# Kernel optimization log

Hardware: AMD Instinct MI355X
Metric: run time of the kernel (lower is better)

## Reference

```python
import jax, jax.numpy as jnp
import numpy as np

N_NODES = 100000
N_EDGES = 3200000
F_IN = 128
HID = 64
N_CLASS = 40


def _glorot(key, shape):
    fan_in, fan_out = shape[1], shape[0]
    s = jnp.sqrt(6.0 / (fan_in + fan_out))
    return jax.random.uniform(key, shape, jnp.float32, -s, s)


def setup_inputs() -> dict:
    key = jax.random.key(0)
    k = jax.random.split(key, 6)
    x = jax.random.normal(k[0], (N_NODES, F_IN), jnp.float32)
    row = jax.random.randint(k[1], (N_EDGES,), 0, N_NODES)
    # guarantee no self loops so add_remaining_self_loops == append all N loops
    off = jax.random.randint(k[2], (N_EDGES,), 1, N_NODES)
    col = (row + off) % N_NODES
    edge_index = jnp.stack([row, col]).astype(jnp.int64)
    y = jax.random.randint(k[3], (N_NODES,), 0, N_CLASS).astype(jnp.int64)
    W1 = _glorot(k[4], (HID, F_IN))
    b1 = jnp.zeros((HID,), jnp.float32)
    W2 = _glorot(k[5], (N_CLASS, HID))
    b2 = jnp.zeros((N_CLASS,), jnp.float32)
    return {"x": x, "edge_index": edge_index, "y": y,
            "W1": W1, "b1": b1, "W2": W2, "b2": b2}


def _gcn_conv(x, edge_index, W, b, num_nodes):
    # append self loops (weight 1.0), per add_remaining_self_loops
    loops = jnp.arange(num_nodes, dtype=edge_index.dtype)
    row = jnp.concatenate([edge_index[0], loops])
    col = jnp.concatenate([edge_index[1], loops])
    w = jnp.ones(row.shape[0], x.dtype)
    # degree-norm: deg over target idx (flow='source_to_target')
    deg = jax.ops.segment_sum(w, col, num_segments=num_nodes)
    dinv = jnp.where(deg > 0, jax.lax.rsqrt(deg), 0.0)
    norm = dinv[row] * w * dinv[col]           # [E+N]
    h = x @ W.T                                # [N, out]
    msg = norm[:, None] * h[row]               # gather + scale
    out = jax.ops.segment_sum(msg, col, num_segments=num_nodes)  # scatter-add
    return out + b


def reference(x, edge_index, y, W1, b1, W2, b2):
    n = x.shape[0]
    h = jax.nn.relu(_gcn_conv(x, edge_index, W1, b1, n))
    # F.dropout treated as identity (eval / deterministic reference)
    x_out = _gcn_conv(h, edge_index, W2, b2, n)
    logp = jax.nn.log_softmax(x_out, axis=1)
    p = jax.nn.softmax(x_out, axis=1)
    pred = jnp.argmax(x_out, axis=1)
    e1 = pred[edge_index[0]]
    e2 = pred[edge_index[1]]
    lab = y[edge_index[0]] == y[edge_index[1]]
    ratio = jnp.mean(((e1 == e2) == lab).astype(jnp.float32))
    return (logp, p, ratio)
```

## Files before the change

kernel.cpp:

```cpp
#include <hip/hip_runtime.h>
#include <hip/hip_fp16.h>

#define N_NODES 100000
#define N_EDGES 3200000
#define F_IN 128
#define HID 64
#define N_CLASS 40
#define ZROW N_NODES

#define NBUCK 196
#define BSHIFT 9
#define NBLK_A 512
#define CHUNK_A ((N_EDGES + NBLK_A - 1) / NBLK_A)

typedef float f32x2 __attribute__((ext_vector_type(2)));

static __device__ __forceinline__ unsigned char enc_fp8(float v) {
    return (unsigned char)(__builtin_amdgcn_cvt_pk_fp8_f32(v, v, 0, false) & 0xff);
}

static __device__ __forceinline__ uint2 gat8(const unsigned char* base, int byteoff, int seg) {
    return *(const uint2*)(base + ((unsigned)byteoff | (unsigned)(seg << 3)));
}

#define CONS(RAW) do { \
    f32x2 f0 = __builtin_amdgcn_cvt_pk_f32_fp8((int)RAW.x, false); \
    f32x2 f1 = __builtin_amdgcn_cvt_pk_f32_fp8((int)RAW.x, true); \
    f32x2 f2 = __builtin_amdgcn_cvt_pk_f32_fp8((int)RAW.y, false); \
    f32x2 f3 = __builtin_amdgcn_cvt_pk_f32_fp8((int)RAW.y, true); \
    a01 += f0; a23 += f1; a45 += f2; a67 += f3; } while (0)

#define SLOTP(s, G, C) { \
    int ib = bb + 6 + s; \
    int srcr = (ib < mydeg) ? C : zb; \
    uint2 ng = gat8(gsrc, srcr, seg); \
    C = sp[min(bb + 12 + s, mlast)]; \
    __builtin_amdgcn_sched_barrier(0); \
    CONS(G); \
    G = ng; }

#define GATHER_PL(TBL) \
    f32x2 a01 = {0.f, 0.f}, a23 = {0.f, 0.f}, a45 = {0.f, 0.f}, a67 = {0.f, 0.f}; \
    { \
        const unsigned char* gsrc = TBL; \
        const int* sp = srow + myoff; \
        const int zb = ZROW << 6; \
        int nbmax = mydeg; \
        nbmax = max(nbmax, __shfl_xor(nbmax, 8)); \
        nbmax = max(nbmax, __shfl_xor(nbmax, 16)); \
        nbmax = max(nbmax, __shfl_xor(nbmax, 32)); \
        if (nbmax > 0) { \
            int mlast = mydeg > 0 ? mydeg - 1 : 0; \
            uint2 g0 = gat8(gsrc, (0 < mydeg) ? sp[0] : zb, seg); \
            uint2 g1 = gat8(gsrc, (1 < mydeg) ? sp[min(1, mlast)] : zb, seg); \
            uint2 g2 = gat8(gsrc, (2 < mydeg) ? sp[min(2, mlast)] : zb, seg); \
            uint2 g3 = gat8(gsrc, (3 < mydeg) ? sp[min(3, mlast)] : zb, seg); \
            uint2 g4 = gat8(gsrc, (4 < mydeg) ? sp[min(4, mlast)] : zb, seg); \
            uint2 g5 = gat8(gsrc, (5 < mydeg) ? sp[min(5, mlast)] : zb, seg); \
            int c0 = sp[min(6, mlast)],  c1 = sp[min(7, mlast)],  c2 = sp[min(8, mlast)]; \
            int c3 = sp[min(9, mlast)], c4 = sp[min(10, mlast)], c5 = sp[min(11, mlast)]; \
            for (int bb = 0; bb < nbmax; bb += 6) { \
                SLOTP(0, g0, c0) SLOTP(1, g1, c1) SLOTP(2, g2, c2) \
                SLOTP(3, g3, c3) SLOTP(4, g4, c4) SLOTP(5, g5, c5) \
            } \
        } \
         \
        uint2 sg = gat8(gsrc, node << 6, seg); \
        CONS(sg); \
    }

__global__ __launch_bounds__(256) void k_A1(const int* __restrict__ col, int* __restrict__ ghistT) {
    __shared__ int hist[256];
    int t = threadIdx.x;
    hist[t] = 0;
    __syncthreads();
    int e0 = blockIdx.x * CHUNK_A;
    int e1 = e0 + CHUNK_A; if (e1 > N_EDGES) e1 = N_EDGES;
    for (int e = e0 + t; e < e1; e += 256) {
        atomicAdd(&hist[col[e] >> BSHIFT], 1);
    }
    __syncthreads();
    ghistT[t * NBLK_A + blockIdx.x] = hist[t];
}

__global__ __launch_bounds__(256) void k_A2a(const int* __restrict__ ghistT, int* __restrict__ goffT,
                                             int* __restrict__ tot) {
    __shared__ int s[256];
    int b = blockIdx.x, t = threadIdx.x;
    int2 v = ((const int2*)(ghistT + b * NBLK_A))[t];
    int pair = v.x + v.y;
    s[t] = pair;
    __syncthreads();
    for (int d = 1; d < 256; d <<= 1) {
        int o = (t >= d) ? s[t - d] : 0;
        __syncthreads();
        s[t] += o;
        __syncthreads();
    }
    int incl = s[t];
    int excl = incl - pair;
    goffT[b * NBLK_A + 2 * t]     = excl;
    goffT[b * NBLK_A + 2 * t + 1] = excl + v.x;
    if (t == 255) tot[b] = incl;
}

__global__ __launch_bounds__(256) void k_A2b(const int* __restrict__ tot, int* __restrict__ bbase,
                                             int* __restrict__ bend,
                                             unsigned char* __restrict__ h1q,
                                             unsigned char* __restrict__ h2q,
                                             const float* __restrict__ b2, float* __restrict__ pb2) {
    __shared__ int s[256];
    int t = threadIdx.x;
    int v = tot[t];
    s[t] = v;
    __syncthreads();
    for (int d = 1; d < 256; d <<= 1) {
        int o = (t >= d) ? s[t - d] : 0;
        __syncthreads();
        s[t] += o;
        __syncthreads();
    }
    bbase[t] = s[t] - v;
    bend[t] = s[t];
    if (t < 64) h1q[(size_t)ZROW * 64 + t] = 0;
    else if (t < 128) h2q[(size_t)ZROW * 64 + (t - 64)] = 0;
    else if (t < 192) pb2[t - 128] = (t - 128 < N_CLASS) ? b2[t - 128] : 0.f;
}

__global__ __launch_bounds__(256) void k_A3(const int* __restrict__ row, const int* __restrict__ col,
                                            const int* __restrict__ goffT, const int* __restrict__ bbase,
                                            unsigned int* __restrict__ epair) {
    __shared__ int cur[256];
    int t = threadIdx.x;
    cur[t] = goffT[t * NBLK_A + blockIdx.x] + bbase[t];
    __syncthreads();
    int e0 = blockIdx.x * CHUNK_A;
    int e1 = e0 + CHUNK_A; if (e1 > N_EDGES) e1 = N_EDGES;
    for (int e = e0 + t; e < e1; e += 256) {
        int c = col[e];
        int pos = atomicAdd(&cur[c >> BSHIFT], 1);
        epair[pos] = ((unsigned int)(c & 511) << 17) | (unsigned int)row[e];
    }
}

__global__ __launch_bounds__(256) void k_B(const unsigned int* __restrict__ epair,
                                           const int* __restrict__ bbase, const int* __restrict__ bend,
                                           int* __restrict__ off, int* __restrict__ pdeg,
                                           float* __restrict__ dinv, int* __restrict__ srow) {
    __shared__ int h[512];
    __shared__ int psc[256];
    int t = threadIdx.x;
    int b = blockIdx.x;
    int n0 = b << BSHIFT;
    int e0 = bbase[b], e1 = bend[b];
    int pbase = e0 + b * 4096;
    h[t] = 0; h[t + 256] = 0;
    __syncthreads();
    for (int e = e0 + t; e < e1; e += 256) {
        atomicAdd(&h[epair[e] >> 17], 1);
    }
    __syncthreads();
    int a0 = h[2 * t], a1 = h[2 * t + 1];
    int p0 = (a0 + 7) & ~7, p1 = (a1 + 7) & ~7;
    psc[t] = p0 + p1;
    __syncthreads();
    for (int d = 1; d < 256; d <<= 1) {
        int o = (t >= d) ? psc[t - d] : 0;
        __syncthreads();
        psc[t] += o;
        __syncthreads();
    }
    int base0 = pbase + psc[t] - (p0 + p1);
    int base1 = base0 + p0;
    h[2 * t] = base0;
    h[2 * t + 1] = base1;
    int n = n0 + 2 * t;
    const int zb = ZROW << 6;
    if (n < N_NODES) {
        off[n] = base0; pdeg[n] = p0; dinv[n] = rsqrtf((float)a0 + 1.0f);
        for (int p = a0; p < p0; ++p) srow[base0 + p] = zb;
    }
    if (n + 1 < N_NODES) {
        off[n + 1] = base1; pdeg[n + 1] = p1; dinv[n + 1] = rsqrtf((float)a1 + 1.0f);
        for (int p = a1; p < p1; ++p) srow[base1 + p] = zb;
    }
    __syncthreads();
    for (int e = e0 + t; e < e1; e += 256) {
        unsigned int k = epair[e];
        int c = k >> 17;
        int pos = atomicAdd(&h[c], 1);
        srow[pos] = (int)(k & 0x1FFFFu) << 6;
    }
}

__global__ __launch_bounds__(256, 4) void k_gemm1(const float* __restrict__ X, const float* __restrict__ W,
                                                  const float* __restrict__ scale, unsigned char* __restrict__ O) {
    __shared__ float wsc[64 * 68];
    __shared__ float xsc[32 * 68];
    int t = threadIdx.x;
    int j = t & 63;
    int r0 = (t >> 6) * 8;
    int rowbase = blockIdx.x * 64;
    float acc[2][8] = {};
#pragma unroll
    for (int kc = 0; kc < 2; ++kc) {
        __syncthreads();
        for (int i4 = t; i4 < 64 * 16; i4 += 256) {
            int jj = i4 >> 4, k4 = i4 & 15;
            float4 v = ((const float4*)W)[jj * 32 + kc * 16 + k4];
            *(float4*)&wsc[jj * 68 + k4 * 4] = v;
        }
#pragma unroll
        for (int chunk = 0; chunk < 2; ++chunk) {
            int cb = rowbase + chunk * 32;
            __syncthreads();
            for (int i4 = t; i4 < 32 * 16; i4 += 256) {
                int r = i4 >> 4, k4 = i4 & 15;
                int rr = cb + r;
                float4 v = make_float4(0.f, 0.f, 0.f, 0.f);
                if (rr < N_NODES) v = ((const float4*)X)[(size_t)rr * 32 + kc * 16 + k4];
                *(float4*)&xsc[r * 68 + k4 * 4] = v;
            }
            __syncthreads();
#pragma unroll 2
            for (int k4 = 0; k4 < 16; ++k4) {
                float4 wv = *(const float4*)&wsc[j * 68 + k4 * 4];
#pragma unroll
                for (int r = 0; r < 8; ++r) {
                    float4 xv = *(const float4*)&xsc[(r0 + r) * 68 + k4 * 4];
                    acc[chunk][r] += xv.x * wv.x + xv.y * wv.y + xv.z * wv.z + xv.w * wv.w;
                }
            }
        }
    }
#pragma unroll
    for (int chunk = 0; chunk < 2; ++chunk) {
#pragma unroll
        for (int r = 0; r < 8; ++r) {
            int rr = rowbase + chunk * 32 + r0 + r;
            if (rr < N_NODES) O[(size_t)rr * 64 + j] = enc_fp8(acc[chunk][r] * scale[rr]);
        }
    }
}

__global__ __launch_bounds__(256, 4) void k_gemm2(const __half* __restrict__ o1h, const float* __restrict__ W2,
                                                  unsigned char* __restrict__ h2q) {
    __shared__ float ws2[N_CLASS * 68];
    __shared__ float xs[32 * 68];
    int t = threadIdx.x;
    for (int i = t; i < N_CLASS * HID; i += 256) {
        int c = i >> 6, k = i & 63;
        ws2[c * 68 + k] = W2[i] * 8.f;
    }
    int j = t & 63;
    int cl = j < N_CLASS ? j : N_CLASS - 1;
    int r0 = (t >> 6) * 8;
    int rowbase = blockIdx.x * 64;
#pragma unroll
    for (int chunk = 0; chunk < 2; ++chunk) {
        int cb = rowbase + chunk * 32;
        __syncthreads();
        {
            int r = t >> 3, k8 = t & 7;
            int rr = cb + r;
            uint4 rawh = make_uint4(0u, 0u, 0u, 0u);
            if (rr < N_NODES) rawh = *(const uint4*)(o1h + (size_t)rr * 64 + k8 * 8);
            __half2* hp = (__half2*)&rawh;
            float2 f0 = __half22float2(hp[0]);
            float2 f1 = __half22float2(hp[1]);
            float2 f2 = __half22float2(hp[2]);
            float2 f3 = __half22float2(hp[3]);
            *(float4*)&xs[r * 68 + k8 * 8]     = make_float4(f0.x, f0.y, f1.x, f1.y);
            *(float4*)&xs[r * 68 + k8 * 8 + 4] = make_float4(f2.x, f2.y, f3.x, f3.y);
        }
        __syncthreads();
        float acc[8] = {0.f, 0.f, 0.f, 0.f, 0.f, 0.f, 0.f, 0.f};
#pragma unroll 2
        for (int k4 = 0; k4 < HID / 4; ++k4) {
            float4 wv = *(const float4*)&ws2[cl * 68 + k4 * 4];
#pragma unroll
            for (int r = 0; r < 8; ++r) {
                float4 xv = *(const float4*)&xs[(r0 + r) * 68 + k4 * 4];
                acc[r] += xv.x * wv.x + xv.y * wv.y + xv.z * wv.z + xv.w * wv.w;
            }
        }
#pragma unroll
        for (int r = 0; r < 8; ++r) {
            int rr = cb + r0 + r;
            if (rr < N_NODES) h2q[(size_t)rr * 64 + j] = (j < N_CLASS) ? enc_fp8(acc[r]) : (unsigned char)0;
        }
    }
}

__global__ __launch_bounds__(256) void k_agg1(const int* __restrict__ off, const int* __restrict__ pdeg,
                                              const int* __restrict__ srow, const float* __restrict__ dinv,
                                              const unsigned char* __restrict__ h1q, const float* __restrict__ b1,
                                              __half* __restrict__ o1h) {
    int t = threadIdx.x;
    int lane = t & 63;
    int e = lane >> 3, seg = lane & 7;
    int node = ((blockIdx.x * 256 + t) >> 6) * 8 + e;
    int myoff = off[node];
    int mydeg = pdeg[node];
    GATHER_PL(h1q)
    float dc = dinv[node];
    float4 ba = *(const float4*)(b1 + seg * 8);
    float4 bb4 = *(const float4*)(b1 + seg * 8 + 4);
    float v0 = dc * a01.x + ba.x,  v1 = dc * a01.y + ba.y;
    float v2 = dc * a23.x + ba.z,  v3 = dc * a23.y + ba.w;
    float v4 = dc * a45.x + bb4.x, v5 = dc * a45.y + bb4.y;
    float v6 = dc * a67.x + bb4.z, v7 = dc * a67.y + bb4.w;
    v0 = v0 > 0.f ? v0 * dc : 0.f; v1 = v1 > 0.f ? v1 * dc : 0.f;
    v2 = v2 > 0.f ? v2 * dc : 0.f; v3 = v3 > 0.f ? v3 * dc : 0.f;
    v4 = v4 > 0.f ? v4 * dc : 0.f; v5 = v5 > 0.f ? v5 * dc : 0.f;
    v6 = v6 > 0.f ? v6 * dc : 0.f; v7 = v7 > 0.f ? v7 * dc : 0.f;
    __half hh[8];
    hh[0] = __float2half(v0); hh[1] = __float2half(v1);
    hh[2] = __float2half(v2); hh[3] = __float2half(v3);
    hh[4] = __float2half(v4); hh[5] = __float2half(v5);
    hh[6] = __float2half(v6); hh[7] = __float2half(v7);
    *(uint4*)(o1h + ((size_t)node * 64 + seg * 8)) = *(uint4*)hh;
}

__global__ __launch_bounds__(256) void k_agg2(const int* __restrict__ off, const int* __restrict__ pdeg,
                                              const int* __restrict__ srow, const float* __restrict__ dinv,
                                              const unsigned char* __restrict__ h2q,
                                              const float* __restrict__ pb2, const int* __restrict__ y,
                                              float* __restrict__ out, unsigned short* __restrict__ ps) {
    int t = threadIdx.x;
    int lane = t & 63;
    int e = lane >> 3, seg = lane & 7;
    int node = ((blockIdx.x * 256 + t) >> 6) * 8 + e;
    int myoff = off[node];
    int mydeg = pdeg[node];
    GATHER_PL(h2q)
    float dc = dinv[node] * 0.125f;
    float4 ba = *(const float4*)(pb2 + seg * 8);
    float4 bb4 = *(const float4*)(pb2 + seg * 8 + 4);
    bool act = seg < 5;
    float v0 = act ? (dc * a01.x + ba.x)  : -1e30f;
    float v1 = act ? (dc * a01.y + ba.y)  : -1e30f;
    float v2 = act ? (dc * a23.x + ba.z)  : -1e30f;
    float v3 = act ? (dc * a23.y + ba.w)  : -1e30f;
    float v4 = act ? (dc * a45.x + bb4.x) : -1e30f;
    float v5 = act ? (dc * a45.y + bb4.y) : -1e30f;
    float v6 = act ? (dc * a67.x + bb4.z) : -1e30f;
    float v7 = act ? (dc * a67.y + bb4.w) : -1e30f;
    float m = v0; int aj = 0;
    if (v1 > m) { m = v1; aj = 1; }
    if (v2 > m) { m = v2; aj = 2; }
    if (v3 > m) { m = v3; aj = 3; }
    if (v4 > m) { m = v4; aj = 4; }
    if (v5 > m) { m = v5; aj = 5; }
    if (v6 > m) { m = v6; aj = 6; }
    if (v7 > m) { m = v7; aj = 7; }
    int ac = seg * 8 + aj;
#pragma unroll
    for (int k = 1; k < 8; k <<= 1) {
        float om = __shfl_xor(m, k);
        int oc = __shfl_xor(ac, k);
        if (om > m || (om == m && oc < ac)) { m = om; ac = oc; }
    }
    float s = 0.f;
    if (act) {
        s = expf(v0 - m) + expf(v1 - m) + expf(v2 - m) + expf(v3 - m)
          + expf(v4 - m) + expf(v5 - m) + expf(v6 - m) + expf(v7 - m);
    }
#pragma unroll
    for (int k = 1; k < 8; k <<= 1) s += __shfl_xor(s, k);
    float ls = logf(s);
    if (act) {
        float lp0 = (v0 - m) - ls, lp1 = (v1 - m) - ls, lp2 = (v2 - m) - ls, lp3 = (v3 - m) - ls;
        float lp4 = (v4 - m) - ls, lp5 = (v5 - m) - ls, lp6 = (v6 - m) - ls, lp7 = (v7 - m) - ls;
        float* logp = out + (size_t)node * N_CLASS + seg * 8;
        *(float4*)logp       = make_float4(lp0, lp1, lp2, lp3);
        *(float4*)(logp + 4) = make_float4(lp4, lp5, lp6, lp7);
        float* pp = out + (size_t)N_NODES * N_CLASS + (size_t)node * N_CLASS + seg * 8;
        *(float4*)pp       = make_float4(expf(lp0), expf(lp1), expf(lp2), expf(lp3));
        *(float4*)(pp + 4) = make_float4(expf(lp4), expf(lp5), expf(lp6), expf(lp7));
    }
    if (seg == 0) ps[node] = (unsigned short)((y[node] << 8) | ac);
}

#define RATIO_BLOCKS 512
__global__ __launch_bounds__(256) void k_ratio(const int* __restrict__ row, const int* __restrict__ col,
                                               const unsigned short* __restrict__ ps,
                                               unsigned int* __restrict__ cnt) {
    const int G = N_EDGES / 8;
    int i = blockIdx.x * 256 + threadIdx.x;
    int stride = RATIO_BLOCKS * 256;
    unsigned int local = 0;
    int e8 = i;
    if (e8 < G) {
        int4 ra = ((const int4*)row)[e8 * 2];
        int4 rb = ((const int4*)row)[e8 * 2 + 1];
        int4 ca = ((const int4*)col)[e8 * 2];
        int4 cb = ((const int4*)col)[e8 * 2 + 1];
        for (;;) {
            int en = e8 + stride;
            bool more = en < G;
            int4 nra, nrb, nca, ncb;
            if (more) {
                nra = ((const int4*)row)[en * 2];
                nrb = ((const int4*)row)[en * 2 + 1];
                nca = ((const int4*)col)[en * 2];
                ncb = ((const int4*)col)[en * 2 + 1];
            }
            unsigned int pa[8], pb[8];
            pa[0] = ps[ra.x]; pa[1] = ps[ra.y]; pa[2] = ps[ra.z]; pa[3] = ps[ra.w];
            pa[4] = ps[rb.x]; pa[5] = ps[rb.y]; pa[6] = ps[rb.z]; pa[7] = ps[rb.w];
            pb[0] = ps[ca.x]; pb[1] = ps[ca.y]; pb[2] = ps[ca.z]; pb[3] = ps[ca.w];
            pb[4] = ps[cb.x]; pb[5] = ps[cb.y]; pb[6] = ps[cb.z]; pb[7] = ps[cb.w];
#pragma unroll
            for (int k = 0; k < 8; ++k) {
                bool sp = (pa[k] & 0xffu) == (pb[k] & 0xffu);
                bool sy = (pa[k] >> 8) == (pb[k] >> 8);
                local += (sp == sy) ? 1u : 0u;
            }
            if (!more) break;
            ra = nra; rb = nrb; ca = nca; cb = ncb;
            e8 = en;
        }
    }
    if (local) atomicAdd(cnt, local);
}

__global__ void k_fin(const unsigned int* __restrict__ cnt, float* __restrict__ out) {
    out[0] = (float)(*cnt) / (float)N_EDGES;
}

extern "C" void kernel_launch(void* const* d_in, const int* in_sizes, int n_in,
                              void* d_out, int out_size, void* d_ws, size_t ws_size,
                              hipStream_t stream) {
    const float* x  = (const float*)d_in[0];
    const int*   ei = (const int*)d_in[1];
    const int*   y  = (const int*)d_in[2];
    const float* W1 = (const float*)d_in[3];
    const float* b1 = (const float*)d_in[4];
    const float* W2 = (const float*)d_in[5];
    const float* b2 = (const float*)d_in[6];

    const int* row = ei;
    const int* col = ei + N_EDGES;

    float* ws = (float*)d_ws;
    unsigned char* h1q = (unsigned char*)ws;
    unsigned char* h2q = (unsigned char*)(ws + 1700000);
    float* dinv   = ws + 3400000;
    int*   pdeg   = (int*)(ws + 3500000);
    int*   off    = (int*)(ws + 3600000);
    int*   srow   = (int*)(ws + 3700000);
    int*   ghistT = (int*)(ws + 7800000);
    int*   goffT  = (int*)(ws + 8000000);
    int*   tot    = (int*)(ws + 8150000);
    int*   bbase  = (int*)(ws + 8200000);
    int*   bend   = (int*)(ws + 8201000);
    float* pb2    = ws + 8202000;
    unsigned short* ps = (unsigned short*)(ws + 8210000);
    unsigned int* cnt  = (unsigned int*)(ws + 8300000);
    unsigned int* epair = (unsigned int*)(ws + 8400000);
    __half* o1h   = (__half*)(ws + 11700000);

    float* out = (float*)d_out;

    (void)hipMemsetAsync(cnt, 0, 4, stream);

    const int GEMM_GRID = (N_NODES + 63) / 64;
    const int AGG_GRID = N_NODES / 32;

    k_A1<<<NBLK_A, 256, 0, stream>>>(col, ghistT);
    k_A2a<<<256, 256, 0, stream>>>(ghistT, goffT, tot);
    k_A2b<<<1, 256, 0, stream>>>(tot, bbase, bend, h1q, h2q, b2, pb2);
    k_A3<<<NBLK_A, 256, 0, stream>>>(row, col, goffT, bbase, epair);
    k_B<<<NBUCK, 256, 0, stream>>>(epair, bbase, bend, off, pdeg, dinv, srow);
    k_gemm1<<<GEMM_GRID, 256, 0, stream>>>(x, W1, dinv, h1q);
    k_agg1<<<AGG_GRID, 256, 0, stream>>>(off, pdeg, srow, dinv, h1q, b1, o1h);
    k_gemm2<<<GEMM_GRID, 256, 0, stream>>>(o1h, W2, h2q);
    k_agg2<<<AGG_GRID, 256, 0, stream>>>(off, pdeg, srow, dinv, h2q, pb2, y, out, ps);
    k_ratio<<<RATIO_BLOCKS, 256, 0, stream>>>(row, col, ps, cnt);
    k_fin<<<1, 1, 0, stream>>>(cnt, out + (size_t)2 * N_NODES * N_CLASS);
}
```

Baseline: 309.2 us.

## Rewrite both dense GEMMs with bf16 MFMA and store hidden activations as bf16

Both node-feature GEMMs now run on MFMA 16x16x32 bf16 instructions. The weights are loaded straight into register fragments, which removes the shared-memory staging and scalar FMA loops. The first aggregation writes its hidden output as bf16 instead of fp16, so the second GEMM can feed it directly into MFMA. The GEMMs are a small part of a pipeline dominated by graph sort and gather, so the overall effect is limited. Precision drops slightly from fp32/fp16 math to bf16 inputs.

```diff
diff --git a/kernel.cpp b/kernel.cpp
--- a/kernel.cpp
+++ b/kernel.cpp
@@ -1,5 +1,4 @@
 #include <hip/hip_runtime.h>
-#include <hip/hip_fp16.h>
 
 #define N_NODES 100000
 #define N_EDGES 3200000
@@ -14,9 +13,16 @@
 #define CHUNK_A ((N_EDGES + NBLK_A - 1) / NBLK_A)
 
 typedef float f32x2 __attribute__((ext_vector_type(2)));
+typedef __attribute__((ext_vector_type(8))) short bf16x8;
+typedef __attribute__((ext_vector_type(4))) float f32x4v;
 
 static __device__ __forceinline__ unsigned char enc_fp8(float v) {
     return (unsigned char)(__builtin_amdgcn_cvt_pk_fp8_f32(v, v, 0, false) & 0xff);
+}
+static __device__ __forceinline__ unsigned cvtpk_bf16(float lo, float hi) {
+    unsigned r;
+    asm("v_cvt_pk_bf16_f32 %0, %1, %2" : "=v"(r) : "v"(lo), "v"(hi));
+    return r;
 }
 
 static __device__ __forceinline__ uint2 gat8(const unsigned char* base, int byteoff, int seg) {
@@ -193,101 +199,105 @@
     }
 }
 
-__global__ __launch_bounds__(256, 4) void k_gemm1(const float* __restrict__ X, const float* __restrict__ W,
-                                                  const float* __restrict__ scale, unsigned char* __restrict__ O) {
-    __shared__ float wsc[64 * 68];
-    __shared__ float xsc[32 * 68];
-    int t = threadIdx.x;
-    int j = t & 63;
-    int r0 = (t >> 6) * 8;
-    int rowbase = blockIdx.x * 64;
-    float acc[2][8] = {};
+#define LDB1(CT, KK, VAR) { \
+    int n = CT * 16 + m; \
+    const float4* p = (const float4*)W + ((size_t)n * 32 + KK * 8 + g * 2); \
+    float4 v0 = p[0], v1 = p[1]; \
+    uint4 u; \
+    u.x = cvtpk_bf16(v0.x, v0.y); u.y = cvtpk_bf16(v0.z, v0.w); \
+    u.z = cvtpk_bf16(v1.x, v1.y); u.w = cvtpk_bf16(v1.z, v1.w); \
+    VAR = *(bf16x8*)&u; }
+
+#define STEP1(KK, B0, B1, B2, B3) { \
+    float4 v0 = make_float4(0.f,0.f,0.f,0.f), v1 = make_float4(0.f,0.f,0.f,0.f); \
+    if (ar < N_NODES) { \
+        const float4* p = (const float4*)X + ((size_t)ar * 32 + KK * 8 + g * 2); \
+        v0 = p[0]; v1 = p[1]; \
+    } \
+    uint4 u; \
+    u.x = cvtpk_bf16(v0.x, v0.y); u.y = cvtpk_bf16(v0.z, v0.w); \
+    u.z = cvtpk_bf16(v1.x, v1.y); u.w = cvtpk_bf16(v1.z, v1.w); \
+    bf16x8 af = *(bf16x8*)&u; \
+    ac0 = __builtin_amdgcn_mfma_f32_16x16x32_bf16(af, B0, ac0, 0, 0, 0); \
+    ac1 = __builtin_amdgcn_mfma_f32_16x16x32_bf16(af, B1, ac1, 0, 0, 0); \
+    ac2 = __builtin_amdgcn_mfma_f32_16x16x32_bf16(af, B2, ac2, 0, 0, 0); \
+    ac3 = __builtin_amdgcn_mfma_f32_16x16x32_bf16(af, B3, ac3, 0, 0, 0); }
+
+__global__ __launch_bounds__(256) void k_gemm1(const float* __restrict__ X, const float* __restrict__ W,
+                                               const float* __restrict__ scale, unsigned char* __restrict__ O) {
+    int t = threadIdx.x;
+    int lane = t & 63, w = t >> 6;
+    int m = lane & 15, g = lane >> 4;
+    bf16x8 b00, b01, b02, b03, b10, b11, b12, b13, b20, b21, b22, b23, b30, b31, b32, b33;
+    LDB1(0,0,b00) LDB1(0,1,b01) LDB1(0,2,b02) LDB1(0,3,b03)
+    LDB1(1,0,b10) LDB1(1,1,b11) LDB1(1,2,b12) LDB1(1,3,b13)
+    LDB1(2,0,b20) LDB1(2,1,b21) LDB1(2,2,b22) LDB1(2,3,b23)
+    LDB1(3,0,b30) LDB1(3,1,b31) LDB1(3,2,b32) LDB1(3,3,b33)
+    int rb = blockIdx.x * 64 + w * 16;
+    int ar = rb + m;
+    f32x4v ac0 = {0.f,0.f,0.f,0.f}, ac1 = {0.f,0.f,0.f,0.f};
+    f32x4v ac2 = {0.f,0.f,0.f,0.f}, ac3 = {0.f,0.f,0.f,0.f};
+    STEP1(0, b00, b10, b20, b30)
+    STEP1(1, b01, b11, b21, b31)
+    STEP1(2, b02, b12, b22, b32)
+    STEP1(3, b03, b13, b23, b33)
 #pragma unroll
-    for (int kc = 0; kc < 2; ++kc) {
-        __syncthreads();
-        for (int i4 = t; i4 < 64 * 16; i4 += 256) {
-            int jj = i4 >> 4, k4 = i4 & 15;
-            float4 v = ((const float4*)W)[jj * 32 + kc * 16 + k4];
-            *(float4*)&wsc[jj * 68 + k4 * 4] = v;
+    for (int r = 0; r < 4; ++r) {
+        int rr = rb + g * 4 + r;
+        if (rr < N_NODES) {
+            float sc = scale[rr];
+            O[(size_t)rr * 64 +      m] = enc_fp8(ac0[r] * sc);
+            O[(size_t)rr * 64 + 16 + m] = enc_fp8(ac1[r] * sc);
+            O[(size_t)rr * 64 + 32 + m] = enc_fp8(ac2[r] * sc);
+            O[(size_t)rr * 64 + 48 + m] = enc_fp8(ac3[r] * sc);
         }
+    }
+}
+
+#define LDB2(CT, KK, VAR) { \
+    int n = CT * 16 + m; \
+    float4 v0 = make_float4(0.f,0.f,0.f,0.f), v1 = make_float4(0.f,0.f,0.f,0.f); \
+    if (n < N_CLASS) { \
+        const float4* p = (const float4*)W2 + ((size_t)n * 16 + KK * 8 + g * 2); \
+        v0 = p[0]; v1 = p[1]; \
+    } \
+    uint4 u; \
+    u.x = cvtpk_bf16(v0.x * 8.f, v0.y * 8.f); u.y = cvtpk_bf16(v0.z * 8.f, v0.w * 8.f); \
+    u.z = cvtpk_bf16(v1.x * 8.f, v1.y * 8.f); u.w = cvtpk_bf16(v1.z * 8.f, v1.w * 8.f); \
+    VAR = *(bf16x8*)&u; }
+
+#define STEP2(KK, B0, B1, B2, B3) { \
+    uint4 u = make_uint4(0u,0u,0u,0u); \
+    if (ar < N_NODES) u = *(const uint4*)(o1b + ((size_t)ar * 64 + KK * 32 + g * 8)); \
+    bf16x8 af = *(bf16x8*)&u; \
+    ac0 = __builtin_amdgcn_mfma_f32_16x16x32_bf16(af, B0, ac0, 0, 0, 0); \
+    ac1 = __builtin_amdgcn_mfma_f32_16x16x32_bf16(af, B1, ac1, 0, 0, 0); \
+    ac2 = __builtin_amdgcn_mfma_f32_16x16x32_bf16(af, B2, ac2, 0, 0, 0); \
+    ac3 = __builtin_amdgcn_mfma_f32_16x16x32_bf16(af, B3, ac3, 0, 0, 0); }
+
+__global__ __launch_bounds__(256) void k_gemm2(const unsigned short* __restrict__ o1b,
+                                               const float* __restrict__ W2,
+                                               unsigned char* __restrict__ h2q) {
+    int t = threadIdx.x;
+    int lane = t & 63, w = t >> 6;
+    int m = lane & 15, g = lane >> 4;
+    bf16x8 b00, b01, b10, b11, b20, b21, b30, b31;
+    LDB2(0,0,b00) LDB2(0,1,b01) LDB2(1,0,b10) LDB2(1,1,b11)
+    LDB2(2,0,b20) LDB2(2,1,b21) LDB2(3,0,b30) LDB2(3,1,b31)
+    int rb = blockIdx.x * 64 + w * 16;
+    int ar = rb + m;
+    f32x4v ac0 = {0.f,0.f,0.f,0.f}, ac1 = {0.f,0.f,0.f,0.f};
+    f32x4v ac2 = {0.f,0.f,0.f,0.f}, ac3 = {0.f,0.f,0.f,0.f};
+    STEP2(0, b00, b10, b20, b30)
+    STEP2(1, b01, b11, b21, b31)
 #pragma unroll
-        for (int chunk = 0; chunk < 2; ++chunk) {
-            int cb = rowbase + chunk * 32;
-            __syncthreads();
-            for (int i4 = t; i4 < 32 * 16; i4 += 256) {
-                int r = i4 >> 4, k4 = i4 & 15;
-                int rr = cb + r;
-                float4 v = make_float4(0.f, 0.f, 0.f, 0.f);
-                if (rr < N_NODES) v = ((const float4*)X)[(size_t)rr * 32 + kc * 16 + k4];
-                *(float4*)&xsc[r * 68 + k4 * 4] = v;
-            }
-            __syncthreads();
-#pragma unroll 2
-            for (int k4 = 0; k4 < 16; ++k4) {
-                float4 wv = *(const float4*)&wsc[j * 68 + k4 * 4];
-#pragma unroll
-                for (int r = 0; r < 8; ++r) {
-                    float4 xv = *(const float4*)&xsc[(r0 + r) * 68 + k4 * 4];
-                    acc[chunk][r] += xv.x * wv.x + xv.y * wv.y + xv.z * wv.z + xv.w * wv.w;
-                }
-            }
-        }
-    }
-#pragma unroll
-    for (int chunk = 0; chunk < 2; ++chunk) {
-#pragma unroll
-        for (int r = 0; r < 8; ++r) {
-            int rr = rowbase + chunk * 32 + r0 + r;
-            if (rr < N_NODES) O[(size_t)rr * 64 + j] = enc_fp8(acc[chunk][r] * scale[rr]);
-        }
-    }
-}
-
-__global__ __launch_bounds__(256, 4) void k_gemm2(const __half* __restrict__ o1h, const float* __restrict__ W2,
-                                                  unsigned char* __restrict__ h2q) {
-    __shared__ float ws2[N_CLASS * 68];
-    __shared__ float xs[32 * 68];
-    int t = threadIdx.x;
-    for (int i = t; i < N_CLASS * HID; i += 256) {
-        int c = i >> 6, k = i & 63;
-        ws2[c * 68 + k] = W2[i] * 8.f;
-    }
-    int j = t & 63;
-    int cl = j < N_CLASS ? j : N_CLASS - 1;
-    int r0 = (t >> 6) * 8;
-    int rowbase = blockIdx.x * 64;
-#pragma unroll
-    for (int chunk = 0; chunk < 2; ++chunk) {
-        int cb = rowbase + chunk * 32;
-        __syncthreads();
-        {
-            int r = t >> 3, k8 = t & 7;
-            int rr = cb + r;
-            uint4 rawh = make_uint4(0u, 0u, 0u, 0u);
-            if (rr < N_NODES) rawh = *(const uint4*)(o1h + (size_t)rr * 64 + k8 * 8);
-            __half2* hp = (__half2*)&rawh;
-            float2 f0 = __half22float2(hp[0]);
-            float2 f1 = __half22float2(hp[1]);
-            float2 f2 = __half22float2(hp[2]);
-            float2 f3 = __half22float2(hp[3]);
-            *(float4*)&xs[r * 68 + k8 * 8]     = make_float4(f0.x, f0.y, f1.x, f1.y);
-            *(float4*)&xs[r * 68 + k8 * 8 + 4] = make_float4(f2.x, f2.y, f3.x, f3.y);
-        }
-        __syncthreads();
-        float acc[8] = {0.f, 0.f, 0.f, 0.f, 0.f, 0.f, 0.f, 0.f};
-#pragma unroll 2
-        for (int k4 = 0; k4 < HID / 4; ++k4) {
-            float4 wv = *(const float4*)&ws2[cl * 68 + k4 * 4];
-#pragma unroll
-            for (int r = 0; r < 8; ++r) {
-                float4 xv = *(const float4*)&xs[(r0 + r) * 68 + k4 * 4];
-                acc[r] += xv.x * wv.x + xv.y * wv.y + xv.z * wv.z + xv.w * wv.w;
-            }
-        }
-#pragma unroll
-        for (int r = 0; r < 8; ++r) {
-            int rr = cb + r0 + r;
-            if (rr < N_NODES) h2q[(size_t)rr * 64 + j] = (j < N_CLASS) ? enc_fp8(acc[r]) : (unsigned char)0;
+    for (int r = 0; r < 4; ++r) {
+        int rr = rb + g * 4 + r;
+        if (rr < N_NODES) {
+            h2q[(size_t)rr * 64 +      m] = enc_fp8(ac0[r]);
+            h2q[(size_t)rr * 64 + 16 + m] = enc_fp8(ac1[r]);
+            h2q[(size_t)rr * 64 + 32 + m] = enc_fp8(ac2[r]);
+            h2q[(size_t)rr * 64 + 48 + m] = enc_fp8(ac3[r]);
         }
     }
 }
@@ -295,7 +305,7 @@
 __global__ __launch_bounds__(256) void k_agg1(const int* __restrict__ off, const int* __restrict__ pdeg,
                                               const int* __restrict__ srow, const float* __restrict__ dinv,
                                               const unsigned char* __restrict__ h1q, const float* __restrict__ b1,
-                                              __half* __restrict__ o1h) {
+                                              unsigned short* __restrict__ o1b) {
     int t = threadIdx.x;
     int lane = t & 63;
     int e = lane >> 3, seg = lane & 7;
@@ -314,12 +324,10 @@
     v2 = v2 > 0.f ? v2 * dc : 0.f; v3 = v3 > 0.f ? v3 * dc : 0.f;
     v4 = v4 > 0.f ? v4 * dc : 0.f; v5 = v5 > 0.f ? v5 * dc : 0.f;
     v6 = v6 > 0.f ? v6 * dc : 0.f; v7 = v7 > 0.f ? v7 * dc : 0.f;
-    __half hh[8];
-    hh[0] = __float2half(v0); hh[1] = __float2half(v1);
-    hh[2] = __float2half(v2); hh[3] = __float2half(v3);
-    hh[4] = __float2half(v4); hh[5] = __float2half(v5);
-    hh[6] = __float2half(v6); hh[7] = __float2half(v7);
-    *(uint4*)(o1h + ((size_t)node * 64 + seg * 8)) = *(uint4*)hh;
+    uint4 pk;
+    pk.x = cvtpk_bf16(v0, v1); pk.y = cvtpk_bf16(v2, v3);
+    pk.z = cvtpk_bf16(v4, v5); pk.w = cvtpk_bf16(v6, v7);
+    *(uint4*)(o1b + ((size_t)node * 64 + seg * 8)) = pk;
 }
 
 __global__ __launch_bounds__(256) void k_agg2(const int* __restrict__ off, const int* __restrict__ pdeg,
@@ -459,7 +467,7 @@
     unsigned short* ps = (unsigned short*)(ws + 8210000);
     unsigned int* cnt  = (unsigned int*)(ws + 8300000);
     unsigned int* epair = (unsigned int*)(ws + 8400000);
-    __half* o1h   = (__half*)(ws + 11700000);
+    unsigned short* o1b = (unsigned short*)(ws + 11700000);
 
     float* out = (float*)d_out;
 
@@ -474,8 +482,8 @@
     k_A3<<<NBLK_A, 256, 0, stream>>>(row, col, goffT, bbase, epair);
     k_B<<<NBUCK, 256, 0, stream>>>(epair, bbase, bend, off, pdeg, dinv, srow);
     k_gemm1<<<GEMM_GRID, 256, 0, stream>>>(x, W1, dinv, h1q);
-    k_agg1<<<AGG_GRID, 256, 0, stream>>>(off, pdeg, srow, dinv, h1q, b1, o1h);
-    k_gemm2<<<GEMM_GRID, 256, 0, stream>>>(o1h, W2, h2q);
+    k_agg1<<<AGG_GRID, 256, 0, stream>>>(off, pdeg, srow, dinv, h1q, b1, o1b);
+    k_gemm2<<<GEMM_GRID, 256, 0, stream>>>(o1b, W2, h2q);
     k_agg2<<<AGG_GRID, 256, 0, stream>>>(off, pdeg, srow, dinv, h2q, pb2, y, out, ps);
     k_ratio<<<RATIO_BLOCKS, 256, 0, stream>>>(row, col, ps, cnt);
     k_fin<<<1, 1, 0, stream>>>(cnt, out + (size_t)2 * N_NODES * N_CLASS);
```

New measurement: 278.4 us. 1.11x faster.
